# Kernel tuning notes

Hardware: AMD Instinct MI355X
Metric: run time of the kernel (lower is better)

Reference implementation:

```python
import jax, jax.numpy as jnp
import numpy as np

L, DIM = 8192, 2048

def setup_inputs() -> dict:
    key = jax.random.key(0)
    k1, k2, k3, k4 = jax.random.split(key, 4)
    x = jax.random.normal(k1, (L, DIM), dtype=jnp.float32)
    x_mix_last = jax.random.normal(k2, (DIM,), dtype=jnp.float32)
    factor_param = jax.random.uniform(k3, (DIM,), dtype=jnp.float32)
    W = jax.random.normal(k4, (DIM, DIM), dtype=jnp.float32) * 0.02
    return {"x": x, "x_mix_last": x_mix_last, "factor_param": factor_param, "W": W}

def reference(x, x_mix_last, factor_param, W):
    # x: [L, D] sequence-first, single sequence (no batch dim, as in the torch module)
    seq_len = x.shape[0]
    factor = jax.nn.sigmoid(factor_param)                       # [D]
    exps = jnp.arange(seq_len)[:, None]                         # [L, 1]
    factor_progression = factor[None, :] ** exps                # [L, D], factor^t
    n = 2 * seq_len
    # FFT-based causal convolution of x with the decay kernel factor^t
    fft_prog = jnp.fft.rfft(factor_progression, n=n, axis=0)    # [L+1, D] complex
    fft_x = jnp.fft.rfft(x, n=n, axis=0)                        # [L+1, D] complex
    conv = jnp.fft.irfft(fft_x * fft_prog, n=n, axis=0)[:seq_len]  # [L, D]
    # EMA update: carry decays as factor^(t+1), new input weighted by (1-factor)
    x_mix = x_mix_last[None, :] * factor_progression * factor[None, :] \
            + (1.0 - factor[None, :]) * conv                    # [L, D]
    return x_mix @ W.T                                          # nn.Linear: x @ W^T
```

## Files before the change

kernel.cpp:

```cpp
#include <hip/hip_runtime.h>

#define L_SEQ 8192
#define DIMN  2048
#define CHUNK 64
#define NCHUNK (L_SEQ / CHUNK)

typedef float  f32x4  __attribute__((ext_vector_type(4)));
typedef __bf16 bf16x8 __attribute__((ext_vector_type(8)));

__device__ __forceinline__ unsigned short f2bf(float f) {
    unsigned int u = __float_as_uint(f);
    u += 0x7fffu + ((u >> 16) & 1u);
    return (unsigned short)(u >> 16);
}

__device__ __forceinline__ float sigmoidf_(float v) {
    return 1.0f / (1.0f + __expf(-v));
}

__global__ void stage1(const float* __restrict__ x, const float* __restrict__ fp,
                       const float* __restrict__ W,
                       float* __restrict__ carry, unsigned short* __restrict__ Wb) {
    int b = blockIdx.x;
    if (b < 256) {
        int cg = b & 1;
        int c  = b >> 1;
        int d4 = cg * 256 + threadIdx.x;
        float4 f4 = ((const float4*)fp)[d4];
        float fa = sigmoidf_(f4.x), fb = sigmoidf_(f4.y),
              fc = sigmoidf_(f4.z), fd = sigmoidf_(f4.w);
        float ga = 1.f - fa, gb = 1.f - fb, gc = 1.f - fc, gd = 1.f - fd;
        float ha = 0.f, hb = 0.f, hc = 0.f, hd = 0.f;
        const float4* xp = (const float4*)(x + (size_t)c * CHUNK * DIMN) + d4;
#pragma unroll 8
        for (int t = 0; t < CHUNK; ++t) {
            float4 v = xp[(size_t)t * (DIMN / 4)];
            ha = fmaf(fa, ha, ga * v.x);
            hb = fmaf(fb, hb, gb * v.y);
            hc = fmaf(fc, hc, gc * v.z);
            hd = fmaf(fd, hd, gd * v.w);
        }
        ((float4*)(carry + (size_t)c * DIMN))[d4] = (float4){ha, hb, hc, hd};
    } else {
        int i = (b - 256) * 256 + threadIdx.x;
        float4 v = ((const float4*)W)[i];
        ushort4 o;
        o.x = f2bf(v.x); o.y = f2bf(v.y); o.z = f2bf(v.z); o.w = f2bf(v.w);
        ((ushort4*)Wb)[i] = o;
    }
}

__global__ __launch_bounds__(64) void carry_prefix(const float* __restrict__ fp,
                                                   const float* __restrict__ xml,
                                                   float* __restrict__ carry) {
    int d = blockIdx.x * 64 + threadIdx.x;
    float f = sigmoidf_(fp[d]);
    float fC = f;
    fC *= fC; fC *= fC; fC *= fC; fC *= fC; fC *= fC; fC *= fC;
    float v[NCHUNK];
#pragma unroll
    for (int c = 0; c < NCHUNK; ++c) v[c] = carry[(size_t)c * DIMN + d];
    float h = xml[d];
#pragma unroll
    for (int c = 0; c < NCHUNK; ++c) {
        carry[(size_t)c * DIMN + d] = h;
        h = fmaf(fC, h, v[c]);
    }
}

__global__ void scan_apply(const float* __restrict__ x, const float* __restrict__ fp,
                           const float* __restrict__ carry, unsigned short* __restrict__ xmix) {
    int b = blockIdx.x;
    int cg = b & 1;
    int c  = b >> 1;
    int d4 = cg * 256 + threadIdx.x;
    float4 f4 = ((const float4*)fp)[d4];
    float fa = sigmoidf_(f4.x), fb = sigmoidf_(f4.y),
          fc = sigmoidf_(f4.z), fd = sigmoidf_(f4.w);
    float ga = 1.f - fa, gb = 1.f - fb, gc = 1.f - fc, gd = 1.f - fd;
    float4 h0 = ((const float4*)(carry + (size_t)c * DIMN))[d4];
    float ha = h0.x, hb = h0.y, hc = h0.z, hd = h0.w;
    const float4* xp = (const float4*)(x + (size_t)c * CHUNK * DIMN) + d4;
    ushort4* op = (ushort4*)(xmix + (size_t)c * CHUNK * DIMN) + d4;
#pragma unroll 8
    for (int t = 0; t < CHUNK; ++t) {
        float4 v = xp[(size_t)t * (DIMN / 4)];
        ha = fmaf(fa, ha, ga * v.x);
        hb = fmaf(fb, hb, gb * v.y);
        hc = fmaf(fc, hc, gc * v.z);
        hd = fmaf(fd, hd, gd * v.w);
        ushort4 o; o.x = f2bf(ha); o.y = f2bf(hb); o.z = f2bf(hc); o.w = f2bf(hd);
        op[(size_t)t * (DIMN / 4)] = o;
    }
}

__global__ __launch_bounds__(256) void gemm_bt(
        const unsigned short* __restrict__ A,
        const unsigned short* __restrict__ B,
        float* __restrict__ C) {
    constexpr int N_ = DIMN, K_ = DIMN;
    constexpr int BK = 64;
    __shared__ __align__(16) unsigned short As[128 * BK];
    __shared__ __align__(16) unsigned short Bs[128 * BK];

    int tid  = threadIdx.x;
    int wave = tid >> 6;
    int lane = tid & 63;
    int quad = lane >> 4;
    int l16  = lane & 15;
    int tm = blockIdx.x, tn = blockIdx.y;
    int wm = wave >> 1, wn = wave & 1;

    f32x4 acc[4][4];
#pragma unroll
    for (int i = 0; i < 4; ++i)
#pragma unroll
        for (int j = 0; j < 4; ++j)
            acc[i][j] = (f32x4){0.f, 0.f, 0.f, 0.f};

    const unsigned short* aBase = A + (size_t)(tm * 128) * K_;
    const unsigned short* bBase = B + (size_t)(tn * 128) * K_;

    for (int k0 = 0; k0 < K_; k0 += BK) {
#pragma unroll
        for (int i = 0; i < 4; ++i) {
            int idx = i * 256 + tid;
            int row = idx >> 3, slot = idx & 7;
            int cc = slot ^ (row & 7);
            __builtin_amdgcn_global_load_lds(
                (const __attribute__((address_space(1))) void*)(aBase + (size_t)row * K_ + k0 + cc * 8),
                (__attribute__((address_space(3))) void*)(As + idx * 8), 16, 0, 0);
        }
#pragma unroll
        for (int i = 0; i < 4; ++i) {
            int idx = i * 256 + tid;
            int row = idx >> 3, slot = idx & 7;
            int cc = slot ^ (row & 7);
            __builtin_amdgcn_global_load_lds(
                (const __attribute__((address_space(1))) void*)(bBase + (size_t)row * K_ + k0 + cc * 8),
                (__attribute__((address_space(3))) void*)(Bs + idx * 8), 16, 0, 0);
        }
        __syncthreads();

#pragma unroll
        for (int kk = 0; kk < BK; kk += 32) {
            bf16x8 af[4], bg[4];
#pragma unroll
            for (int i = 0; i < 4; ++i) {
                int r = wm * 64 + i * 16 + l16;
                int c0 = (kk >> 3) + quad;
                af[i] = *(const bf16x8*)(As + r * BK + ((c0 ^ (r & 7)) << 3));
            }
#pragma unroll
            for (int j = 0; j < 4; ++j) {
                int r = wn * 64 + j * 16 + l16;
                int c0 = (kk >> 3) + quad;
                bg[j] = *(const bf16x8*)(Bs + r * BK + ((c0 ^ (r & 7)) << 3));
            }
#pragma unroll
            for (int i = 0; i < 4; ++i)
#pragma unroll
                for (int j = 0; j < 4; ++j)
                    acc[i][j] = __builtin_amdgcn_mfma_f32_16x16x32_bf16(af[i], bg[j], acc[i][j], 0, 0, 0);
        }
        __syncthreads();
    }

#pragma unroll
    for (int i = 0; i < 4; ++i) {
#pragma unroll
        for (int j = 0; j < 4; ++j) {
            int col = tn * 128 + wn * 64 + j * 16 + l16;
#pragma unroll
            for (int r = 0; r < 4; ++r) {
                int row = tm * 128 + wm * 64 + i * 16 + quad * 4 + r;
                C[(size_t)row * N_ + col] = acc[i][j][r];
            }
        }
    }
}

extern "C" void kernel_launch(void* const* d_in, const int* in_sizes, int n_in,
                              void* d_out, int out_size, void* d_ws, size_t ws_size,
                              hipStream_t stream) {
    const float* x   = (const float*)d_in[0];
    const float* xml = (const float*)d_in[1];
    const float* fp  = (const float*)d_in[2];
    const float* W   = (const float*)d_in[3];
    float* out = (float*)d_out;

    unsigned short* xmix = (unsigned short*)d_ws;
    unsigned short* Wb   = (unsigned short*)((char*)d_ws + (size_t)L_SEQ * DIMN * 2);
    float* carry = (float*)((char*)d_ws + (size_t)L_SEQ * DIMN * 2 + (size_t)DIMN * DIMN * 2);

    stage1<<<256 + DIMN * DIMN / 4 / 256, 256, 0, stream>>>(x, fp, W, carry, Wb);
    carry_prefix<<<DIMN / 64, 64, 0, stream>>>(fp, xml, carry);
    scan_apply<<<256, 256, 0, stream>>>(x, fp, carry, xmix);
    gemm_bt<<<dim3(L_SEQ / 128, DIMN / 128), 256, 0, stream>>>(xmix, Wb, out);
}
```

Baseline: 221.6 us.

## Write local scan in stage1 and add carry correction pass instead of rescanning x

The first pass now stores the chunk-local scan result to xmix in bf16, so x is read only once. A light correction pass then adds carry*f^t to the stored values, replacing the full second scan over x. Chunk size is halved to give more blocks, the weight conversion is batched per block, and the GEMM grid is reordered so consecutive blocks share A tiles. The correction reads and rewrites xmix through bf16, which adds a second rounding step and slightly reduces precision.

```diff
diff --git a/kernel.cpp b/kernel.cpp
--- a/kernel.cpp
+++ b/kernel.cpp
@@ -2,7 +2,7 @@
 
 #define L_SEQ 8192
 #define DIMN  2048
-#define CHUNK 64
+#define CHUNK 32
 #define NCHUNK (L_SEQ / CHUNK)
 
 typedef float  f32x4  __attribute__((ext_vector_type(4)));
@@ -13,16 +13,19 @@
     u += 0x7fffu + ((u >> 16) & 1u);
     return (unsigned short)(u >> 16);
 }
-
+__device__ __forceinline__ float bf2f(unsigned short u) {
+    return __uint_as_float((unsigned int)u << 16);
+}
 __device__ __forceinline__ float sigmoidf_(float v) {
     return 1.0f / (1.0f + __expf(-v));
 }
 
 __global__ void stage1(const float* __restrict__ x, const float* __restrict__ fp,
                        const float* __restrict__ W,
-                       float* __restrict__ carry, unsigned short* __restrict__ Wb) {
+                       float* __restrict__ carryA, unsigned short* __restrict__ xmix,
+                       unsigned short* __restrict__ Wb) {
     int b = blockIdx.x;
-    if (b < 256) {
+    if (b < 512) {
         int cg = b & 1;
         int c  = b >> 1;
         int d4 = cg * 256 + threadIdx.x;
@@ -31,7 +34,8 @@
               fc = sigmoidf_(f4.z), fd = sigmoidf_(f4.w);
         float ga = 1.f - fa, gb = 1.f - fb, gc = 1.f - fc, gd = 1.f - fd;
         float ha = 0.f, hb = 0.f, hc = 0.f, hd = 0.f;
-        const float4* xp = (const float4*)(x + (size_t)c * CHUNK * DIMN) + d4;
+        const float4* xp = (const float4*)x + (size_t)c * CHUNK * (DIMN / 4) + d4;
+        ushort4* lp = (ushort4*)xmix + (size_t)c * CHUNK * (DIMN / 4) + d4;
 #pragma unroll 8
         for (int t = 0; t < CHUNK; ++t) {
             float4 v = xp[(size_t)t * (DIMN / 4)];
@@ -39,37 +43,39 @@
             hb = fmaf(fb, hb, gb * v.y);
             hc = fmaf(fc, hc, gc * v.z);
             hd = fmaf(fd, hd, gd * v.w);
-        }
-        ((float4*)(carry + (size_t)c * DIMN))[d4] = (float4){ha, hb, hc, hd};
+            ushort4 o; o.x = f2bf(ha); o.y = f2bf(hb); o.z = f2bf(hc); o.w = f2bf(hd);
+            lp[(size_t)t * (DIMN / 4)] = o;
+        }
+        ((float4*)(carryA + (size_t)c * DIMN))[d4] = (float4){ha, hb, hc, hd};
     } else {
-        int i = (b - 256) * 256 + threadIdx.x;
-        float4 v = ((const float4*)W)[i];
-        ushort4 o;
-        o.x = f2bf(v.x); o.y = f2bf(v.y); o.z = f2bf(v.z); o.w = f2bf(v.w);
-        ((ushort4*)Wb)[i] = o;
-    }
-}
-
-__global__ __launch_bounds__(64) void carry_prefix(const float* __restrict__ fp,
-                                                   const float* __restrict__ xml,
-                                                   float* __restrict__ carry) {
-    int d = blockIdx.x * 64 + threadIdx.x;
+#pragma unroll
+        for (int k = 0; k < 8; ++k) {
+            int i = (b - 512) * 2048 + k * 256 + threadIdx.x;
+            float4 v = ((const float4*)W)[i];
+            ushort4 o;
+            o.x = f2bf(v.x); o.y = f2bf(v.y); o.z = f2bf(v.z); o.w = f2bf(v.w);
+            ((ushort4*)Wb)[i] = o;
+        }
+    }
+}
+
+__global__ void carry_prefix(const float* __restrict__ fp, const float* __restrict__ xml,
+                             const float* __restrict__ carryA, float* __restrict__ carryB) {
+    int d = blockIdx.x * 256 + threadIdx.x;
     float f = sigmoidf_(fp[d]);
     float fC = f;
-    fC *= fC; fC *= fC; fC *= fC; fC *= fC; fC *= fC; fC *= fC;
-    float v[NCHUNK];
-#pragma unroll
-    for (int c = 0; c < NCHUNK; ++c) v[c] = carry[(size_t)c * DIMN + d];
+    fC *= fC; fC *= fC; fC *= fC; fC *= fC; fC *= fC;
     float h = xml[d];
-#pragma unroll
+#pragma unroll 8
     for (int c = 0; c < NCHUNK; ++c) {
-        carry[(size_t)c * DIMN + d] = h;
-        h = fmaf(fC, h, v[c]);
-    }
-}
-
-__global__ void scan_apply(const float* __restrict__ x, const float* __restrict__ fp,
-                           const float* __restrict__ carry, unsigned short* __restrict__ xmix) {
+        float lv = carryA[(size_t)c * DIMN + d];
+        carryB[(size_t)c * DIMN + d] = h;
+        h = fmaf(fC, h, lv);
+    }
+}
+
+__global__ void apply_corr(const float* __restrict__ fp, const float* __restrict__ carryB,
+                           unsigned short* __restrict__ xmix) {
     int b = blockIdx.x;
     int cg = b & 1;
     int c  = b >> 1;
@@ -77,20 +83,19 @@
     float4 f4 = ((const float4*)fp)[d4];
     float fa = sigmoidf_(f4.x), fb = sigmoidf_(f4.y),
           fc = sigmoidf_(f4.z), fd = sigmoidf_(f4.w);
-    float ga = 1.f - fa, gb = 1.f - fb, gc = 1.f - fc, gd = 1.f - fd;
-    float4 h0 = ((const float4*)(carry + (size_t)c * DIMN))[d4];
-    float ha = h0.x, hb = h0.y, hc = h0.z, hd = h0.w;
-    const float4* xp = (const float4*)(x + (size_t)c * CHUNK * DIMN) + d4;
-    ushort4* op = (ushort4*)(xmix + (size_t)c * CHUNK * DIMN) + d4;
+    float4 H = ((const float4*)(carryB + (size_t)c * DIMN))[d4];
+    float pa = fa, pb = fb, pc = fc, pd = fd;
+    ushort4* lp = (ushort4*)xmix + (size_t)c * CHUNK * (DIMN / 4) + d4;
 #pragma unroll 8
     for (int t = 0; t < CHUNK; ++t) {
-        float4 v = xp[(size_t)t * (DIMN / 4)];
-        ha = fmaf(fa, ha, ga * v.x);
-        hb = fmaf(fb, hb, gb * v.y);
-        hc = fmaf(fc, hc, gc * v.z);
-        hd = fmaf(fd, hd, gd * v.w);
-        ushort4 o; o.x = f2bf(ha); o.y = f2bf(hb); o.z = f2bf(hc); o.w = f2bf(hd);
-        op[(size_t)t * (DIMN / 4)] = o;
+        ushort4 u = lp[(size_t)t * (DIMN / 4)];
+        ushort4 o;
+        o.x = f2bf(fmaf(H.x, pa, bf2f(u.x)));
+        o.y = f2bf(fmaf(H.y, pb, bf2f(u.y)));
+        o.z = f2bf(fmaf(H.z, pc, bf2f(u.z)));
+        o.w = f2bf(fmaf(H.w, pd, bf2f(u.w)));
+        lp[(size_t)t * (DIMN / 4)] = o;
+        pa *= fa; pb *= fb; pc *= fc; pd *= fd;
     }
 }
 
@@ -108,7 +113,7 @@
     int lane = tid & 63;
     int quad = lane >> 4;
     int l16  = lane & 15;
-    int tm = blockIdx.x, tn = blockIdx.y;
+    int tn = blockIdx.x, tm = blockIdx.y;
     int wm = wave >> 1, wn = wave & 1;
 
     f32x4 acc[4][4];
@@ -191,10 +196,11 @@
 
     unsigned short* xmix = (unsigned short*)d_ws;
     unsigned short* Wb   = (unsigned short*)((char*)d_ws + (size_t)L_SEQ * DIMN * 2);
-    float* carry = (float*)((char*)d_ws + (size_t)L_SEQ * DIMN * 2 + (size_t)DIMN * DIMN * 2);
-
-    stage1<<<256 + DIMN * DIMN / 4 / 256, 256, 0, stream>>>(x, fp, W, carry, Wb);
-    carry_prefix<<<DIMN / 64, 64, 0, stream>>>(fp, xml, carry);
-    scan_apply<<<256, 256, 0, stream>>>(x, fp, carry, xmix);
-    gemm_bt<<<dim3(L_SEQ / 128, DIMN / 128), 256, 0, stream>>>(xmix, Wb, out);
-}
+    float* carryA = (float*)((char*)d_ws + 40ull * 1024 * 1024);
+    float* carryB = (float*)((char*)d_ws + 42ull * 1024 * 1024);
+
+    stage1<<<1024, 256, 0, stream>>>(x, fp, W, carryA, xmix, Wb);
+    carry_prefix<<<DIMN / 256, 256, 0, stream>>>(fp, xml, carryA, carryB);
+    apply_corr<<<512, 256, 0, stream>>>(fp, carryB, xmix);
+    gemm_bt<<<dim3(DIMN / 128, L_SEQ / 128), 256, 0, stream>>>(xmix, Wb, out);
+}
```

Result: slower. 246.7 us (+11.3%).
